# Performance work log

Hardware: AMD Instinct MI355X
Metric: run time of the kernel (lower is better)

## Reference

```python
import jax, jax.numpy as jnp
import numpy as np

NUM_CAPSULE = 32
DIM_CAPSULE = 32
ROUTINGS = 3
T_EPSILON = 1e-7


def setup_inputs() -> dict:
    key = jax.random.key(0)
    k1, k2 = jax.random.split(key)
    x = jax.random.normal(k1, (64, 1024, 256), dtype=jnp.float32)
    # xavier_normal_ on [1, 256, 32*32]: std = sqrt(2/(fan_in+fan_out)) = sqrt(2/(256+1024))
    std = np.sqrt(2.0 / (256 + NUM_CAPSULE * DIM_CAPSULE)).astype(np.float32)
    W = jax.random.normal(k2, (1, 256, NUM_CAPSULE * DIM_CAPSULE), dtype=jnp.float32) * std
    return {"x": x, "W": W}


def _squash(v, eps):
    # x / sqrt(sum(x^2) + eps)  (note: not the classic squash; faithful to source)
    s = jnp.sum(v * v, axis=-1, keepdims=True)
    return v / jnp.sqrt(s + eps)


def reference(x, W):
    B, N_in, _ = x.shape
    # u_hat: [B, num_capsule, input_num_capsule, dim_capsule]
    u_hat = jnp.matmul(x, W).reshape(B, N_in, NUM_CAPSULE, DIM_CAPSULE)
    u_hat = jnp.transpose(u_hat, (0, 2, 1, 3))
    b = jnp.zeros(u_hat.shape[:3], dtype=u_hat.dtype)  # [B, num, n_in]
    outputs = None
    for i in range(ROUTINGS):
        # original: softmax over the num_capsule axis (dim=2 after permute(0,2,1))
        c = jax.nn.softmax(b, axis=1)  # [B, num, n_in]
        outputs = _squash(jnp.einsum('bij,bijk->bik', c, u_hat), T_EPSILON)  # [B, num, dim]
        if i < ROUTINGS - 1:
            b = jnp.einsum('bik,bijk->bij', outputs, u_hat)
    return outputs
```

## Files before the change

kernel.cpp:

```cpp
#include <hip/hip_runtime.h>
#include <cstdint>
#include <cstddef>

#define BATCH 64
#define NIN   1024
#define CIN   256
#define NC    32
#define NJC   16
#define JCH   64
#define NP0   8
#define T_EPS 1e-7f

#define WTS_S 264
#define XT_S  72
#define CT_S  72

typedef __attribute__((ext_vector_type(8))) short short8;
typedef __attribute__((ext_vector_type(4))) float floatx4;

__device__ __forceinline__ unsigned short bf16rne(float f) {
  unsigned int u = __float_as_uint(f);
  u += 0x7FFFu + ((u >> 16) & 1u);
  return (unsigned short)(u >> 16);
}
__device__ __forceinline__ float bf2f(unsigned short h) {
  return __uint_as_float(((unsigned int)h) << 16);
}

__global__ __launch_bounds__(256) void k_convert(const float* __restrict__ x,
                                                 unsigned short* __restrict__ xb,
                                                 float* __restrict__ y0p) {
  const int b = blockIdx.y, g = blockIdx.x, t = threadIdx.x;
  const size_t base = ((size_t)(b * NIN + g * 128)) * CIN + t;
  const float* xp = x + base;
  unsigned short* xo = xb + base;
  float acc = 0.f;
  #pragma unroll 8
  for (int j = 0; j < 128; ++j) {
    float v = xp[(size_t)j * CIN];
    acc += v;
    xo[(size_t)j * CIN] = bf16rne(v);
  }
  y0p[(b * NP0 + g) * CIN + t] = acc;
}

template <int MODE>
__global__ __launch_bounds__(256) void k_post(const void* __restrict__ yin,
                                              const float* __restrict__ W,
                                              unsigned short* __restrict__ wtout,
                                              float* __restrict__ outg) {
  const int i = blockIdx.x, b = blockIdx.y, t = threadIdx.x;
  __shared__ float Wl[CIN][36];
  __shared__ float ys[CIN];
  __shared__ float sred[8][32];
  __shared__ float os[NC];
  const float4* W4 = (const float4*)W;
  #pragma unroll
  for (int q = 0; q < 8; ++q) {
    int f = q * 256 + t;
    int c = f >> 3, k4 = f & 7;
    float4 v = W4[c * (NC * 8) + i * 8 + k4];
    *(float4*)&Wl[c][k4 * 4] = v;
  }
  float a = 0.f;
  if (MODE == 0) {
    const float* y0p = (const float*)yin;
    #pragma unroll
    for (int p = 0; p < NP0; ++p) a += y0p[(b * NP0 + p) * CIN + t];
    a *= (1.f / 32.f);
  } else {
    const unsigned short* yp = (const unsigned short*)yin;
    #pragma unroll
    for (int p = 0; p < NJC; ++p)
      a += bf2f(yp[(((size_t)(b * NJC + p)) * NC + i) * CIN + t]);
  }
  ys[t] = a;
  __syncthreads();
  {
    const int k = t & 31, g = t >> 5;
    float ps = 0.f;
    #pragma unroll
    for (int cc = 0; cc < 32; ++cc) {
      int c = g * 32 + cc;
      ps += ys[c] * Wl[c][k];
    }
    sred[g][k] = ps;
  }
  __syncthreads();
  const int k = t & 31;
  float s = 0.f;
  #pragma unroll
  for (int g = 0; g < 8; ++g) s += sred[g][k];
  float s2 = s * s;
  #pragma unroll
  for (int m = 1; m < 32; m <<= 1) s2 += __shfl_xor(s2, m);
  float o = s * rsqrtf(s2 + T_EPS);
  if (MODE == 2) {
    if (t < 32) outg[((size_t)b * NC + i) * 32 + t] = o;
  } else {
    if (t < 32) os[t] = o;
    __syncthreads();
    const int rot = ((t >> 3) & 7) * 4;
    float acc = 0.f;
    #pragma unroll
    for (int kkk = 0; kkk < 32; ++kkk) {
      int kk = (kkk + rot) & 31;
      acc += Wl[t][kk] * os[kk];
    }
    wtout[((size_t)b * NC + i) * CIN + t] = bf16rne(acc);
  }
}

__global__ __launch_bounds__(256) void k_fused(const unsigned short* __restrict__ xb,
                                               const unsigned short* __restrict__ wt,
                                               unsigned short* __restrict__ ypart) {
  const int jc = blockIdx.x, b = blockIdx.y, t = threadIdx.x;
  const int w = t >> 6, lane = t & 63;
  const int l16 = lane & 15, q = lane >> 4;
  __shared__ unsigned short wts[NC * WTS_S];
  __shared__ unsigned short xT[CIN * XT_S];
  __shared__ unsigned short cT[NC * CT_S];
  {
    const ushort4* wg = (const ushort4*)(wt + (size_t)b * NC * CIN);
    #pragma unroll
    for (int it = 0; it < 8; ++it) {
      int f = it * 256 + t;
      int i = f >> 6, o4 = f & 63;
      *(ushort4*)&wts[i * WTS_S + o4 * 4] = wg[f];
    }
  }
  const int jloc = w * 16 + l16;
  const unsigned short* xrow =
      xb + ((size_t)(b * NIN) + (size_t)jc * JCH + jloc) * CIN;
  short8 bfr[2];
  bfr[0] = *(const short8*)(xrow + 0 * 32 + q * 8);
  bfr[1] = *(const short8*)(xrow + 1 * 32 + q * 8);
  floatx4 accA0 = {0.f, 0.f, 0.f, 0.f}, accA1 = {0.f, 0.f, 0.f, 0.f};
  __syncthreads();
  #pragma unroll
  for (int ks = 0; ks < 8; ++ks) {
    short8 bcur = bfr[ks & 1];
    if (ks < 6) bfr[ks & 1] = *(const short8*)(xrow + (ks + 2) * 32 + q * 8);
    short8 a0 = *(const short8*)&wts[l16 * WTS_S + ks * 32 + q * 8];
    short8 a1 = *(const short8*)&wts[(16 + l16) * WTS_S + ks * 32 + q * 8];
    accA0 = __builtin_amdgcn_mfma_f32_16x16x32_bf16(a0, bcur, accA0, 0, 0, 0);
    accA1 = __builtin_amdgcn_mfma_f32_16x16x32_bf16(a1, bcur, accA1, 0, 0, 0);
    #pragma unroll
    for (int e = 0; e < 8; ++e) {
      int c = ks * 32 + q * 8 + e;
      xT[c * XT_S + jloc] = (unsigned short)bcur[e];
    }
  }
  {
    float m = accA0[0];
    #pragma unroll
    for (int r = 1; r < 4; ++r) m = fmaxf(m, accA0[r]);
    #pragma unroll
    for (int r = 0; r < 4; ++r) m = fmaxf(m, accA1[r]);
    m = fmaxf(m, __shfl_xor(m, 16));
    m = fmaxf(m, __shfl_xor(m, 32));
    float e0[4], e1[4], s = 0.f;
    #pragma unroll
    for (int r = 0; r < 4; ++r) {
      e0[r] = __expf(accA0[r] - m);
      e1[r] = __expf(accA1[r] - m);
      s += e0[r] + e1[r];
    }
    s += __shfl_xor(s, 16);
    s += __shfl_xor(s, 32);
    float rs = 1.f / s;
    #pragma unroll
    for (int r = 0; r < 4; ++r) {
      cT[(q * 4 + r) * CT_S + jloc]        = bf16rne(e0[r] * rs);
      cT[(16 + q * 4 + r) * CT_S + jloc]   = bf16rne(e1[r] * rs);
    }
  }
  __syncthreads();
  const int cw = w * 64;
  floatx4 accB[2][4];
  #pragma unroll
  for (int it = 0; it < 2; ++it)
    #pragma unroll
    for (int ct = 0; ct < 4; ++ct) accB[it][ct] = (floatx4){0.f, 0.f, 0.f, 0.f};
  #pragma unroll
  for (int ks = 0; ks < 2; ++ks) {
    short8 ca0 = *(const short8*)&cT[l16 * CT_S + ks * 32 + q * 8];
    short8 ca1 = *(const short8*)&cT[(16 + l16) * CT_S + ks * 32 + q * 8];
    #pragma unroll
    for (int ct = 0; ct < 4; ++ct) {
      short8 xf = *(const short8*)&xT[(cw + ct * 16 + l16) * XT_S + ks * 32 + q * 8];
      accB[0][ct] = __builtin_amdgcn_mfma_f32_16x16x32_bf16(ca0, xf, accB[0][ct], 0, 0, 0);
      accB[1][ct] = __builtin_amdgcn_mfma_f32_16x16x32_bf16(ca1, xf, accB[1][ct], 0, 0, 0);
    }
  }
  unsigned short* yo = ypart + ((size_t)(b * NJC + jc)) * NC * CIN;
  #pragma unroll
  for (int it = 0; it < 2; ++it)
    #pragma unroll
    for (int ct = 0; ct < 4; ++ct)
      #pragma unroll
      for (int r = 0; r < 4; ++r) {
        int i = it * 16 + q * 4 + r;
        int c = cw + ct * 16 + l16;
        yo[i * CIN + c] = bf16rne(accB[it][ct][r]);
      }
}

extern "C" void kernel_launch(void* const* d_in, const int* in_sizes, int n_in,
                              void* d_out, int out_size, void* d_ws, size_t ws_size,
                              hipStream_t stream) {
  (void)in_sizes; (void)n_in; (void)out_size; (void)ws_size;
  const float* x = (const float*)d_in[0];
  const float* W = (const float*)d_in[1];
  float* out = (float*)d_out;
  char* ws = (char*)d_ws;
  unsigned short* xbuf  = (unsigned short*)ws;
  unsigned short* wtb   = (unsigned short*)(ws + (34ull << 20));
  unsigned short* ypart = (unsigned short*)(ws + (35ull << 20));
  float*          y0p   = (float*)(ws + (52ull << 20));

  dim3 gconv(NP0, BATCH);
  dim3 gfuse(NJC, BATCH);
  dim3 gpost(NC, BATCH);
  k_convert<<<gconv, 256, 0, stream>>>(x, xbuf, y0p);
  k_post<0><<<gpost, 256, 0, stream>>>(y0p, W, wtb, nullptr);
  k_fused<<<gfuse, 256, 0, stream>>>(xbuf, wtb, ypart);
  k_post<1><<<gpost, 256, 0, stream>>>(ypart, W, wtb, nullptr);
  k_fused<<<gfuse, 256, 0, stream>>>(xbuf, wtb, ypart);
  k_post<2><<<gpost, 256, 0, stream>>>(ypart, W, nullptr, out);
}
```

Measured before the change: 156.4 us.

## Precompute transposed bf16 x chunks in convert kernel; drop LDS staging in fused kernel

The convert kernel now also writes a per-chunk transposed bf16 copy of x, built through shared memory, and uses 16 chunks per batch. The fused routing kernel reads W^T rows and the transposed x directly from global memory instead of staging them in LDS. This cuts LDS use, which allows launch bounds of 4 blocks per CU, and removes the in-kernel transpose scatter. The cost is an extra 32MB write of x and a second global read of it in each fused pass, plus uncoalesced-style short8 global loads of the weights.

```diff
diff --git a/kernel.cpp b/kernel.cpp
--- a/kernel.cpp
+++ b/kernel.cpp
@@ -8,12 +8,9 @@
 #define NC    32
 #define NJC   16
 #define JCH   64
-#define NP0   8
 #define T_EPS 1e-7f
-
-#define WTS_S 264
-#define XT_S  72
 #define CT_S  72
+#define XT_SS 68
 
 typedef __attribute__((ext_vector_type(8))) short short8;
 typedef __attribute__((ext_vector_type(4))) float floatx4;
@@ -29,19 +26,29 @@
 
 __global__ __launch_bounds__(256) void k_convert(const float* __restrict__ x,
                                                  unsigned short* __restrict__ xb,
+                                                 unsigned short* __restrict__ xbT,
                                                  float* __restrict__ y0p) {
-  const int b = blockIdx.y, g = blockIdx.x, t = threadIdx.x;
-  const size_t base = ((size_t)(b * NIN + g * 128)) * CIN + t;
-  const float* xp = x + base;
-  unsigned short* xo = xb + base;
+  const int jc = blockIdx.x, b = blockIdx.y, t = threadIdx.x;
+  __shared__ unsigned short xsT[CIN * XT_SS];
+  const size_t base = ((size_t)(b * NIN + jc * JCH)) * CIN;
   float acc = 0.f;
   #pragma unroll 8
-  for (int j = 0; j < 128; ++j) {
-    float v = xp[(size_t)j * CIN];
+  for (int j = 0; j < JCH; ++j) {
+    float v = x[base + (size_t)j * CIN + t];
     acc += v;
-    xo[(size_t)j * CIN] = bf16rne(v);
-  }
-  y0p[(b * NP0 + g) * CIN + t] = acc;
+    unsigned short h = bf16rne(v);
+    xb[base + (size_t)j * CIN + t] = h;
+    xsT[t * XT_SS + j] = h;
+  }
+  y0p[(b * NJC + jc) * CIN + t] = acc;
+  __syncthreads();
+  ushort4* dstv = (ushort4*)(xbT + (size_t)(b * NJC + jc) * (CIN * JCH));
+  #pragma unroll
+  for (int it = 0; it < 16; ++it) {
+    int f = it * 256 + t;
+    int c = f >> 4, j4 = f & 15;
+    dstv[f] = *(const ushort4*)&xsT[c * XT_SS + j4 * 4];
+  }
 }
 
 template <int MODE>
@@ -66,7 +73,7 @@
   if (MODE == 0) {
     const float* y0p = (const float*)yin;
     #pragma unroll
-    for (int p = 0; p < NP0; ++p) a += y0p[(b * NP0 + p) * CIN + t];
+    for (int p = 0; p < NJC; ++p) a += y0p[(b * NJC + p) * CIN + t];
     a *= (1.f / 32.f);
   } else {
     const unsigned short* yp = (const unsigned short*)yin;
@@ -111,45 +118,25 @@
   }
 }
 
-__global__ __launch_bounds__(256) void k_fused(const unsigned short* __restrict__ xb,
-                                               const unsigned short* __restrict__ wt,
-                                               unsigned short* __restrict__ ypart) {
+__global__ __launch_bounds__(256, 4) void k_fused(const unsigned short* __restrict__ xb,
+                                                  const unsigned short* __restrict__ xbT,
+                                                  const unsigned short* __restrict__ wt,
+                                                  unsigned short* __restrict__ ypart) {
   const int jc = blockIdx.x, b = blockIdx.y, t = threadIdx.x;
-  const int w = t >> 6, lane = t & 63;
-  const int l16 = lane & 15, q = lane >> 4;
-  __shared__ unsigned short wts[NC * WTS_S];
-  __shared__ unsigned short xT[CIN * XT_S];
+  const int w = t >> 6, l16 = t & 15, q = (t >> 4) & 3;
   __shared__ unsigned short cT[NC * CT_S];
-  {
-    const ushort4* wg = (const ushort4*)(wt + (size_t)b * NC * CIN);
-    #pragma unroll
-    for (int it = 0; it < 8; ++it) {
-      int f = it * 256 + t;
-      int i = f >> 6, o4 = f & 63;
-      *(ushort4*)&wts[i * WTS_S + o4 * 4] = wg[f];
-    }
-  }
   const int jloc = w * 16 + l16;
   const unsigned short* xrow =
       xb + ((size_t)(b * NIN) + (size_t)jc * JCH + jloc) * CIN;
-  short8 bfr[2];
-  bfr[0] = *(const short8*)(xrow + 0 * 32 + q * 8);
-  bfr[1] = *(const short8*)(xrow + 1 * 32 + q * 8);
+  const unsigned short* wrow = wt + (size_t)b * NC * CIN;
   floatx4 accA0 = {0.f, 0.f, 0.f, 0.f}, accA1 = {0.f, 0.f, 0.f, 0.f};
-  __syncthreads();
   #pragma unroll
   for (int ks = 0; ks < 8; ++ks) {
-    short8 bcur = bfr[ks & 1];
-    if (ks < 6) bfr[ks & 1] = *(const short8*)(xrow + (ks + 2) * 32 + q * 8);
-    short8 a0 = *(const short8*)&wts[l16 * WTS_S + ks * 32 + q * 8];
-    short8 a1 = *(const short8*)&wts[(16 + l16) * WTS_S + ks * 32 + q * 8];
-    accA0 = __builtin_amdgcn_mfma_f32_16x16x32_bf16(a0, bcur, accA0, 0, 0, 0);
-    accA1 = __builtin_amdgcn_mfma_f32_16x16x32_bf16(a1, bcur, accA1, 0, 0, 0);
-    #pragma unroll
-    for (int e = 0; e < 8; ++e) {
-      int c = ks * 32 + q * 8 + e;
-      xT[c * XT_S + jloc] = (unsigned short)bcur[e];
-    }
+    short8 bx = *(const short8*)(xrow + ks * 32 + q * 8);
+    short8 a0 = *(const short8*)(wrow + (size_t)l16 * CIN + ks * 32 + q * 8);
+    short8 a1 = *(const short8*)(wrow + (size_t)(16 + l16) * CIN + ks * 32 + q * 8);
+    accA0 = __builtin_amdgcn_mfma_f32_16x16x32_bf16(a0, bx, accA0, 0, 0, 0);
+    accA1 = __builtin_amdgcn_mfma_f32_16x16x32_bf16(a1, bx, accA1, 0, 0, 0);
   }
   {
     float m = accA0[0];
@@ -171,38 +158,39 @@
     float rs = 1.f / s;
     #pragma unroll
     for (int r = 0; r < 4; ++r) {
-      cT[(q * 4 + r) * CT_S + jloc]        = bf16rne(e0[r] * rs);
-      cT[(16 + q * 4 + r) * CT_S + jloc]   = bf16rne(e1[r] * rs);
+      cT[(q * 4 + r) * CT_S + jloc]      = bf16rne(e0[r] * rs);
+      cT[(16 + q * 4 + r) * CT_S + jloc] = bf16rne(e1[r] * rs);
     }
   }
   __syncthreads();
   const int cw = w * 64;
+  const unsigned short* xTb = xbT + (size_t)(b * NJC + jc) * (CIN * JCH);
   floatx4 accB[2][4];
   #pragma unroll
-  for (int it = 0; it < 2; ++it)
-    #pragma unroll
-    for (int ct = 0; ct < 4; ++ct) accB[it][ct] = (floatx4){0.f, 0.f, 0.f, 0.f};
+  for (int h = 0; h < 2; ++h)
+    #pragma unroll
+    for (int ct = 0; ct < 4; ++ct) accB[h][ct] = (floatx4){0.f, 0.f, 0.f, 0.f};
   #pragma unroll
   for (int ks = 0; ks < 2; ++ks) {
     short8 ca0 = *(const short8*)&cT[l16 * CT_S + ks * 32 + q * 8];
     short8 ca1 = *(const short8*)&cT[(16 + l16) * CT_S + ks * 32 + q * 8];
     #pragma unroll
     for (int ct = 0; ct < 4; ++ct) {
-      short8 xf = *(const short8*)&xT[(cw + ct * 16 + l16) * XT_S + ks * 32 + q * 8];
+      short8 xf = *(const short8*)(xTb + (size_t)(cw + ct * 16 + l16) * JCH + ks * 32 + q * 8);
       accB[0][ct] = __builtin_amdgcn_mfma_f32_16x16x32_bf16(ca0, xf, accB[0][ct], 0, 0, 0);
       accB[1][ct] = __builtin_amdgcn_mfma_f32_16x16x32_bf16(ca1, xf, accB[1][ct], 0, 0, 0);
     }
   }
   unsigned short* yo = ypart + ((size_t)(b * NJC + jc)) * NC * CIN;
   #pragma unroll
-  for (int it = 0; it < 2; ++it)
+  for (int h = 0; h < 2; ++h)
     #pragma unroll
     for (int ct = 0; ct < 4; ++ct)
       #pragma unroll
       for (int r = 0; r < 4; ++r) {
-        int i = it * 16 + q * 4 + r;
+        int i = h * 16 + q * 4 + r;
         int c = cw + ct * 16 + l16;
-        yo[i * CIN + c] = bf16rne(accB[it][ct][r]);
+        yo[i * CIN + c] = bf16rne(accB[h][ct][r]);
       }
 }
 
@@ -215,17 +203,17 @@
   float* out = (float*)d_out;
   char* ws = (char*)d_ws;
   unsigned short* xbuf  = (unsigned short*)ws;
-  unsigned short* wtb   = (unsigned short*)(ws + (34ull << 20));
-  unsigned short* ypart = (unsigned short*)(ws + (35ull << 20));
-  float*          y0p   = (float*)(ws + (52ull << 20));
-
-  dim3 gconv(NP0, BATCH);
+  unsigned short* xbufT = (unsigned short*)(ws + (32ull << 20));
+  unsigned short* wtb   = (unsigned short*)(ws + (64ull << 20));
+  unsigned short* ypart = (unsigned short*)(ws + (65ull << 20));
+  float*          y0p   = (float*)(ws + (81ull << 20));
+
   dim3 gfuse(NJC, BATCH);
   dim3 gpost(NC, BATCH);
-  k_convert<<<gconv, 256, 0, stream>>>(x, xbuf, y0p);
+  k_convert<<<gfuse, 256, 0, stream>>>(x, xbuf, xbufT, y0p);
   k_post<0><<<gpost, 256, 0, stream>>>(y0p, W, wtb, nullptr);
-  k_fused<<<gfuse, 256, 0, stream>>>(xbuf, wtb, ypart);
+  k_fused<<<gfuse, 256, 0, stream>>>(xbuf, xbufT, wtb, ypart);
   k_post<1><<<gpost, 256, 0, stream>>>(ypart, W, wtb, nullptr);
-  k_fused<<<gfuse, 256, 0, stream>>>(xbuf, wtb, ypart);
+  k_fused<<<gfuse, 256, 0, stream>>>(xbuf, xbufT, wtb, ypart);
   k_post<2><<<gpost, 256, 0, stream>>>(ypart, W, nullptr, out);
 }
```

New measurement: 172.2 us. 1.1x slower.
